# Optimization experiments

Hardware: AMD Instinct MI355X
Metric: run time of the kernel (lower is better)

## Reference

```python
import jax, jax.numpy as jnp
import numpy as np

N_NODES = 100000
N_EDGES = 3200000
N_GRAPHS = 64
NODE_FEATS = 32
LATENT = [32, 32, 32, 1]
OUT_DIM = 128
TOTAL_LATENT = sum(LATENT)  # 97


def setup_inputs() -> dict:
    key = jax.random.key(0)
    ks = jax.random.split(key, 16)
    node_feat = jax.random.normal(ks[0], (N_NODES, NODE_FEATS), dtype=jnp.float32)
    src = jax.random.randint(ks[1], (N_EDGES,), 0, N_NODES)
    dst = jax.random.randint(ks[2], (N_EDGES,), 0, N_NODES)
    graph_ids = jnp.sort(jax.random.randint(ks[3], (N_NODES,), 0, N_GRAPHS))
    # layer weights: Linear(in, out) -> W [in, out], b [out]
    dims = [NODE_FEATS] + LATENT
    inp = {
        'node_feat': node_feat,
        'src': src,
        'dst': dst,
        'graph_ids': graph_ids,
        'num_graphs': N_GRAPHS,
    }
    for i in range(len(LATENT)):
        inp[f'W{i}'] = 0.1 * jax.random.normal(ks[4 + 2 * i], (dims[i], dims[i + 1]), dtype=jnp.float32)
        inp[f'b{i}'] = 0.1 * jax.random.normal(ks[5 + 2 * i], (dims[i + 1],), dtype=jnp.float32)
    inp['Wout'] = 0.1 * jax.random.normal(ks[12], (TOTAL_LATENT, OUT_DIM), dtype=jnp.float32)
    inp['bout'] = 0.1 * jax.random.normal(ks[13], (OUT_DIM,), dtype=jnp.float32)
    return inp


def reference(node_feat, W0, b0, W1, b1, W2, b2, W3, b3, Wout, bout,
              src, dst, graph_ids, num_graphs):
    N = node_feat.shape[0]
    # node_degs = deg + 1 (adjacency row sums + 1)
    degs = jax.ops.segment_sum(jnp.ones_like(dst, dtype=node_feat.dtype), dst, num_segments=N)
    node_degs = (degs + 1.0)[:, None]  # [N, 1]

    params = [(W0, b0), (W1, b1), (W2, b2), (W3, b3)]
    h = node_feat
    cats = []
    for W, b in params:
        # n2npool = A @ h + h  (sparse SpMM via edge-list segment sum)
        agg = jax.ops.segment_sum(h[src], dst, num_segments=N) + h
        h = jnp.tanh((agg @ W + b) / node_degs)
        cats.append(h)
    hcat = jnp.concatenate(cats, axis=1)  # [N, 97]

    # per-graph sum pooling
    pooled = jax.ops.segment_sum(hcat, graph_ids, num_segments=num_graphs)  # [G, 97]
    # relu(relu(linear)) == relu(linear)
    out = jax.nn.relu(pooled @ Wout + bout)
    return out
```

## Files before the change

### kernel.cpp

```cpp
#include <hip/hip_runtime.h>
#include <hip/hip_bf16.h>


#define NFEAT 32
#define TOTLAT 97
#define NGRAPH 64
#define OUTDIM 128
#define BSHIFT 9
#define NPB 512
#define MAXBUCK 256
#define CH 8192

__device__ __forceinline__ float ftanh(float x) {
    x = fminf(fmaxf(x, -15.0f), 15.0f);
    float t = __expf(2.0f * x);
    return (t - 1.0f) / (t + 1.0f);
}

__global__ __launch_bounds__(256) void hist_kernel(const int* __restrict__ dst,
                                                   int* __restrict__ bucket_cnt,
                                                   int E, int nbuck) {
    __shared__ int h[MAXBUCK];
    for (int i = threadIdx.x; i < nbuck; i += blockDim.x) h[i] = 0;
    __syncthreads();
    int e0 = blockIdx.x * CH, e1 = min(e0 + CH, E);
    const int4* d4 = (const int4*)dst;
    int k0 = e0 >> 2, nk = (e1 - e0) >> 2;
    for (int k = k0 + threadIdx.x; k < k0 + nk; k += blockDim.x) {
        int4 v = d4[k];
        atomicAdd(&h[v.x >> BSHIFT], 1);
        atomicAdd(&h[v.y >> BSHIFT], 1);
        atomicAdd(&h[v.z >> BSHIFT], 1);
        atomicAdd(&h[v.w >> BSHIFT], 1);
    }
    for (int e = e0 + (nk << 2) + threadIdx.x; e < e1; e += blockDim.x)
        atomicAdd(&h[dst[e] >> BSHIFT], 1);
    __syncthreads();
    for (int i = threadIdx.x; i < nbuck; i += blockDim.x)
        if (h[i]) atomicAdd(&bucket_cnt[i], h[i]);
}

__global__ void bucket_scan_kernel(const int* __restrict__ bucket_cnt,
                                   int* __restrict__ bucket_start,
                                   int* __restrict__ bucket_cursor,
                                   int* __restrict__ row_ptr,
                                   int N, int E, int nbuck) {
    __shared__ int s[MAXBUCK];
    int i = threadIdx.x;
    int v = (i < nbuck) ? bucket_cnt[i] : 0;
    s[i] = v;
    __syncthreads();
    for (int d = 1; d < MAXBUCK; d <<= 1) {
        int t = (i >= d) ? s[i - d] : 0;
        __syncthreads();
        if (i >= d) s[i] += t;
        __syncthreads();
    }
    if (i < nbuck) {
        int excl = s[i] - v;
        bucket_start[i] = excl;
        bucket_cursor[i] = excl;
    }
    if (i == 0) { bucket_start[nbuck] = E; row_ptr[N] = E; }
}

__global__ __launch_bounds__(256) void part_kernel(const int* __restrict__ src,
                                                   const int* __restrict__ dst,
                                                   int* __restrict__ bucket_cursor,
                                                   int2* __restrict__ pairs,
                                                   int E, int nbuck) {
    __shared__ int h[MAXBUCK];
    __shared__ int gb[MAXBUCK];
    for (int i = threadIdx.x; i < nbuck; i += blockDim.x) h[i] = 0;
    __syncthreads();
    int e0 = blockIdx.x * CH, e1 = min(e0 + CH, E);
    const int4* d4 = (const int4*)dst;
    const int4* s4 = (const int4*)src;
    int k0 = e0 >> 2, nk = (e1 - e0) >> 2;
    for (int k = k0 + threadIdx.x; k < k0 + nk; k += blockDim.x) {
        int4 v = d4[k];
        atomicAdd(&h[v.x >> BSHIFT], 1);
        atomicAdd(&h[v.y >> BSHIFT], 1);
        atomicAdd(&h[v.z >> BSHIFT], 1);
        atomicAdd(&h[v.w >> BSHIFT], 1);
    }
    for (int e = e0 + (nk << 2) + threadIdx.x; e < e1; e += blockDim.x)
        atomicAdd(&h[dst[e] >> BSHIFT], 1);
    __syncthreads();
    for (int i = threadIdx.x; i < nbuck; i += blockDim.x) {
        int c = h[i];
        gb[i] = c ? atomicAdd(&bucket_cursor[i], c) : 0;
        h[i] = 0;
    }
    __syncthreads();
    for (int k = k0 + threadIdx.x; k < k0 + nk; k += blockDim.x) {
        int4 d = d4[k];
        int4 s = s4[k];
        int b, r;
        b = d.x >> BSHIFT; r = atomicAdd(&h[b], 1); pairs[gb[b] + r] = make_int2(s.x, d.x);
        b = d.y >> BSHIFT; r = atomicAdd(&h[b], 1); pairs[gb[b] + r] = make_int2(s.y, d.y);
        b = d.z >> BSHIFT; r = atomicAdd(&h[b], 1); pairs[gb[b] + r] = make_int2(s.z, d.z);
        b = d.w >> BSHIFT; r = atomicAdd(&h[b], 1); pairs[gb[b] + r] = make_int2(s.w, d.w);
    }
    for (int e = e0 + (nk << 2) + threadIdx.x; e < e1; e += blockDim.x) {
        int dv = dst[e];
        int b = dv >> BSHIFT;
        int r = atomicAdd(&h[b], 1);
        pairs[gb[b] + r] = make_int2(src[e], dv);
    }
}

__global__ __launch_bounds__(NPB) void csr_kernel(const int2* __restrict__ pairs,
                                                  const int* __restrict__ bucket_start,
                                                  int* __restrict__ row_ptr,
                                                  int* __restrict__ col_idx,
                                                  float* __restrict__ inv_deg, int N) {
    __shared__ int deg[NPB];
    __shared__ int scn[NPB];
    int b = blockIdx.x;
    int n0 = b << BSHIFT;
    int tid = threadIdx.x;
    deg[tid] = 0;
    __syncthreads();
    int e0 = bucket_start[b], e1 = bucket_start[b + 1];
    for (int e = e0 + tid; e < e1; e += NPB) {
        int2 p = pairs[e];
        atomicAdd(&deg[p.y - n0], 1);
    }
    __syncthreads();
    int v = deg[tid];
    scn[tid] = v;
    __syncthreads();
    for (int d = 1; d < NPB; d <<= 1) {
        int t = (tid >= d) ? scn[tid - d] : 0;
        __syncthreads();
        if (tid >= d) scn[tid] += t;
        __syncthreads();
    }
    int excl = scn[tid] - v;
    int n = n0 + tid;
    if (n < N) {
        row_ptr[n] = e0 + excl;
        inv_deg[n] = 1.0f / ((float)v + 1.0f);
    }
    deg[tid] = excl;
    __syncthreads();
    for (int e = e0 + tid; e < e1; e += NPB) {
        int2 p = pairs[e];
        int r = atomicAdd(&deg[p.y - n0], 1);
        col_idx[e0 + r] = p.x;
    }
}

template <bool WRITE_Y>
__global__ __launch_bounds__(256, 8) void layer_fused(
    const float* __restrict__ h_in, float* __restrict__ h_out,
    const float* __restrict__ W, const float* __restrict__ bvec,
    const int* __restrict__ row_ptr, const int* __restrict__ col_idx,
    const float* __restrict__ inv_deg,
    const float* __restrict__ W3, float* __restrict__ y, int N)
{
    __shared__ float accs[32][33];
    const int t = blockIdx.x * blockDim.x + threadIdx.x;
    int n = t >> 3;
    const int l8 = t & 7;
    const bool valid = n < N;
    if (!valid) n = N - 1;

    const float4* __restrict__ h4 = (const float4*)h_in;

    int beg = row_ptr[n];
    int end = row_ptr[n + 1];
    int len = end - beg;
    float4 self = h4[(size_t)n * 8 + l8];
    float4 acc = self;

    for (int e = beg; e < end; e += 32) {
        int base = e + l8 * 4;
        int my0 = __builtin_nontemporal_load(&col_idx[base + 0]);
        int my1 = __builtin_nontemporal_load(&col_idx[base + 1]);
        int my2 = __builtin_nontemporal_load(&col_idx[base + 2]);
        int my3 = __builtin_nontemporal_load(&col_idx[base + 3]);
        int rem = end - e;
#pragma unroll
        for (int sl = 0; sl < 8; ++sl) {
            int i0 = __shfl(my0, sl, 8);
            int i1 = __shfl(my1, sl, 8);
            int i2 = __shfl(my2, sl, 8);
            int i3 = __shfl(my3, sl, 8);
            int j = sl * 4;
            i0 = (j + 0 < rem) ? i0 : n;
            i1 = (j + 1 < rem) ? i1 : n;
            i2 = (j + 2 < rem) ? i2 : n;
            i3 = (j + 3 < rem) ? i3 : n;
            float4 v0 = h4[(size_t)i0 * 8 + l8];
            float4 v1 = h4[(size_t)i1 * 8 + l8];
            float4 v2 = h4[(size_t)i2 * 8 + l8];
            float4 v3 = h4[(size_t)i3 * 8 + l8];
            acc.x += v0.x + v1.x + v2.x + v3.x;
            acc.y += v0.y + v1.y + v2.y + v3.y;
            acc.z += v0.z + v1.z + v2.z + v3.z;
            acc.w += v0.w + v1.w + v2.w + v3.w;
        }
    }
    float fk = (float)(((len + 31) & ~31) - len);
    acc.x -= fk * self.x; acc.y -= fk * self.y;
    acc.z -= fk * self.z; acc.w -= fk * self.w;

    const int gl = threadIdx.x >> 3;
    const int f0 = l8 * 4;
    accs[gl][f0 + 0] = acc.x;
    accs[gl][f0 + 1] = acc.y;
    accs[gl][f0 + 2] = acc.z;
    accs[gl][f0 + 3] = acc.w;

    float4 o = *(const float4*)&bvec[f0];
#pragma unroll 8
    for (int k = 0; k < NFEAT; ++k) {
        float a = accs[gl][k];
        float4 w = *(const float4*)&W[k * NFEAT + f0];
        o.x += a * w.x; o.y += a * w.y; o.z += a * w.z; o.w += a * w.w;
    }
    float ideg = inv_deg[n];
    float4 v;
    v.x = ftanh(o.x * ideg);
    v.y = ftanh(o.y * ideg);
    v.z = ftanh(o.z * ideg);
    v.w = ftanh(o.w * ideg);

    if (valid) {
        *(float4*)&h_out[(size_t)n * NFEAT + f0] = v;
        if (WRITE_Y) {
            float4 wv = *(const float4*)&W3[f0];
            float p = v.x * wv.x + v.y * wv.y + v.z * wv.z + v.w * wv.w;
            p += __shfl_xor(p, 1);
            p += __shfl_xor(p, 2);
            p += __shfl_xor(p, 4);
            if (l8 == 0) y[n] = p;
        }
    }
}

__global__ __launch_bounds__(256) void agg3_kernel(
    const float* __restrict__ y, const float* __restrict__ b3,
    const int* __restrict__ row_ptr, const int* __restrict__ col_idx,
    const float* __restrict__ inv_deg, float* __restrict__ z, int N)
{
    int n = blockIdx.x * blockDim.x + threadIdx.x;
    if (n >= N) return;

    int beg = row_ptr[n];
    int end = row_ptr[n + 1];
    float s = y[n];
    int e = beg;
    for (; e + 8 <= end; e += 8) {
        float a0 = y[col_idx[e + 0]];
        float a1 = y[col_idx[e + 1]];
        float a2 = y[col_idx[e + 2]];
        float a3 = y[col_idx[e + 3]];
        float a4 = y[col_idx[e + 4]];
        float a5 = y[col_idx[e + 5]];
        float a6 = y[col_idx[e + 6]];
        float a7 = y[col_idx[e + 7]];
        s += ((a0 + a1) + (a2 + a3)) + ((a4 + a5) + (a6 + a7));
    }
    for (; e < end; ++e)
        s += y[col_idx[e]];

    z[n] = ftanh((s + b3[0]) * inv_deg[n]);
}

__global__ __launch_bounds__(128) void pool_kernel(
    const float* __restrict__ h0, const float* __restrict__ h1,
    const float* __restrict__ h2, const float* __restrict__ z,
    const int* __restrict__ graph_ids, float* __restrict__ pooled, int N)
{
    __shared__ int sb[2];
    int g = blockIdx.x >> 2, q = blockIdx.x & 3;
    if (threadIdx.x == 0) {
        int lo = 0, hi = N;
        while (lo < hi) { int m = (lo + hi) >> 1; if (graph_ids[m] < g) lo = m + 1; else hi = m; }
        sb[0] = lo;
        lo = 0; hi = N;
        while (lo < hi) { int m = (lo + hi) >> 1; if (graph_ids[m] < g + 1) lo = m + 1; else hi = m; }
        sb[1] = lo;
    }
    __syncthreads();
    int s = sb[0], e = sb[1];
    int per = (e - s + 3) >> 2;
    int ns = s + q * per;
    int ne = min(ns + per, e);
    int c = threadIdx.x;
    if (c >= TOTLAT || ns >= ne) return;

    float sum = 0.0f;
    if (c < 32) {
        const float* p = h0 + c;
#pragma unroll 4
        for (int n = ns; n < ne; ++n) sum += p[(size_t)n * NFEAT];
    } else if (c < 64) {
        const float* p = h1 + (c - 32);
#pragma unroll 4
        for (int n = ns; n < ne; ++n) sum += p[(size_t)n * NFEAT];
    } else if (c < 96) {
        const float* p = h2 + (c - 64);
#pragma unroll 4
        for (int n = ns; n < ne; ++n) sum += p[(size_t)n * NFEAT];
    } else {
#pragma unroll 4
        for (int n = ns; n < ne; ++n) sum += z[n];
    }
    atomicAdd(&pooled[g * TOTLAT + c], sum);
}

__global__ void final_kernel(const float* __restrict__ pooled, const float* __restrict__ Wout,
                             const float* __restrict__ bout, float* __restrict__ out) {
    int g = blockIdx.x;
    int o = threadIdx.x;
    float s = bout[o];
#pragma unroll 4
    for (int k = 0; k < TOTLAT; ++k)
        s += pooled[g * TOTLAT + k] * Wout[k * OUTDIM + o];
    out[g * OUTDIM + o] = fmaxf(s, 0.0f);
}

extern "C" void kernel_launch(void* const* d_in, const int* in_sizes, int n_in,
                              void* d_out, int out_size, void* d_ws, size_t ws_size,
                              hipStream_t stream) {
    const float* node_feat = (const float*)d_in[0];
    const int*   src       = (const int*)d_in[1];
    const int*   dst       = (const int*)d_in[2];
    const int*   graph_ids = (const int*)d_in[3];
    const float* W0 = (const float*)d_in[5];
    const float* b0 = (const float*)d_in[6];
    const float* W1 = (const float*)d_in[7];
    const float* b1 = (const float*)d_in[8];
    const float* W2 = (const float*)d_in[9];
    const float* b2 = (const float*)d_in[10];
    const float* W3 = (const float*)d_in[11];
    const float* b3 = (const float*)d_in[12];
    const float* Wout = (const float*)d_in[13];
    const float* bout = (const float*)d_in[14];
    float* out = (float*)d_out;

    const int N = in_sizes[0] / NFEAT;
    const int E = in_sizes[1];
    const int nbuck = (N + NPB - 1) >> BSHIFT;

    char* ws = (char*)d_ws;
    size_t off = 0;
    auto carve = [&](size_t bytes) -> void* {
        void* p = ws + off;
        off = (off + bytes + 255) & ~(size_t)255;
        return p;
    };
    int*   bucket_cnt    = (int*)carve((size_t)MAXBUCK * 4);
    int*   bucket_start  = (int*)carve((size_t)(MAXBUCK + 1) * 4);
    int*   bucket_cursor = (int*)carve((size_t)MAXBUCK * 4);
    int*   row_ptr       = (int*)carve((size_t)(N + 1) * 4);
    int*   col_idx       = (int*)carve((size_t)(E + 32) * 4);
    float* inv_deg       = (float*)carve((size_t)N * 4);
    float* hA            = (float*)carve((size_t)N * NFEAT * 4);
    float* hB            = (float*)carve((size_t)N * NFEAT * 4);
    float* hC            = (float*)carve((size_t)N * NFEAT * 4);
    float* y             = (float*)carve((size_t)N * 4);
    float* z             = (float*)carve((size_t)N * 4);
    float* pooled        = (float*)carve((size_t)NGRAPH * TOTLAT * 4);
    int2*  pairs         = (int2*)hA;

    hipMemsetAsync(bucket_cnt, 0, (size_t)MAXBUCK * 4, stream);
    hipMemsetAsync(pooled, 0, (size_t)NGRAPH * TOTLAT * 4, stream);

    const int nchunks = (E + CH - 1) / CH;
    hist_kernel<<<nchunks, 256, 0, stream>>>(dst, bucket_cnt, E, nbuck);
    bucket_scan_kernel<<<1, MAXBUCK, 0, stream>>>(bucket_cnt, bucket_start, bucket_cursor,
                                                  row_ptr, N, E, nbuck);
    part_kernel<<<nchunks, 256, 0, stream>>>(src, dst, bucket_cursor, pairs, E, nbuck);
    csr_kernel<<<nbuck, NPB, 0, stream>>>(pairs, bucket_start, row_ptr, col_idx, inv_deg, N);

    const int lblocks = (N * 8 + 255) / 256;
    layer_fused<false><<<lblocks, 256, 0, stream>>>(node_feat, hA, W0, b0, row_ptr, col_idx,
                                                    inv_deg, nullptr, nullptr, N);
    layer_fused<false><<<lblocks, 256, 0, stream>>>(hA, hB, W1, b1, row_ptr, col_idx,
                                                    inv_deg, nullptr, nullptr, N);
    layer_fused<true><<<lblocks, 256, 0, stream>>>(hB, hC, W2, b2, row_ptr, col_idx,
                                                   inv_deg, W3, y, N);
    agg3_kernel<<<(N + 255) / 256, 256, 0, stream>>>(y, b3, row_ptr, col_idx, inv_deg, z, N);

    pool_kernel<<<NGRAPH * 4, 128, 0, stream>>>(hA, hB, hC, z, graph_ids, pooled, N);
    final_kernel<<<NGRAPH, OUTDIM, 0, stream>>>(pooled, Wout, bout, out);
}
```

Before: 520.5 us.

## Gather neighbor features in bf16 and pack edge pairs into 32-bit words

```diff
diff --git a/kernel.cpp b/kernel.cpp
--- a/kernel.cpp
+++ b/kernel.cpp
@@ -15,6 +15,23 @@
     x = fminf(fmaxf(x, -15.0f), 15.0f);
     float t = __expf(2.0f * x);
     return (t - 1.0f) / (t + 1.0f);
+}
+__device__ __forceinline__ unsigned short f2b(float f) {
+    unsigned int x = __float_as_uint(f);
+    return (unsigned short)((x + 0x7FFFu + ((x >> 16) & 1u)) >> 16);
+}
+__device__ __forceinline__ float b2f(unsigned short u) {
+    return __uint_as_float(((unsigned int)u) << 16);
+}
+
+__global__ __launch_bounds__(256) void conv_kernel(const float* __restrict__ in,
+                                                   unsigned short* __restrict__ outb, int total4) {
+    int i = blockIdx.x * blockDim.x + threadIdx.x;
+    if (i >= total4) return;
+    float4 v = ((const float4*)in)[i];
+    ushort4 o;
+    o.x = f2b(v.x); o.y = f2b(v.y); o.z = f2b(v.z); o.w = f2b(v.w);
+    ((ushort4*)outb)[i] = o;
 }
 
 __global__ __launch_bounds__(256) void hist_kernel(const int* __restrict__ dst,
@@ -67,7 +84,7 @@
 __global__ __launch_bounds__(256) void part_kernel(const int* __restrict__ src,
                                                    const int* __restrict__ dst,
                                                    int* __restrict__ bucket_cursor,
-                                                   int2* __restrict__ pairs,
+                                                   int* __restrict__ pairs,
                                                    int E, int nbuck) {
     __shared__ int h[MAXBUCK];
     __shared__ int gb[MAXBUCK];
@@ -97,20 +114,20 @@
         int4 d = d4[k];
         int4 s = s4[k];
         int b, r;
-        b = d.x >> BSHIFT; r = atomicAdd(&h[b], 1); pairs[gb[b] + r] = make_int2(s.x, d.x);
-        b = d.y >> BSHIFT; r = atomicAdd(&h[b], 1); pairs[gb[b] + r] = make_int2(s.y, d.y);
-        b = d.z >> BSHIFT; r = atomicAdd(&h[b], 1); pairs[gb[b] + r] = make_int2(s.z, d.z);
-        b = d.w >> BSHIFT; r = atomicAdd(&h[b], 1); pairs[gb[b] + r] = make_int2(s.w, d.w);
+        b = d.x >> BSHIFT; r = atomicAdd(&h[b], 1); pairs[gb[b] + r] = s.x | ((d.x & 511) << 17);
+        b = d.y >> BSHIFT; r = atomicAdd(&h[b], 1); pairs[gb[b] + r] = s.y | ((d.y & 511) << 17);
+        b = d.z >> BSHIFT; r = atomicAdd(&h[b], 1); pairs[gb[b] + r] = s.z | ((d.z & 511) << 17);
+        b = d.w >> BSHIFT; r = atomicAdd(&h[b], 1); pairs[gb[b] + r] = s.w | ((d.w & 511) << 17);
     }
     for (int e = e0 + (nk << 2) + threadIdx.x; e < e1; e += blockDim.x) {
         int dv = dst[e];
         int b = dv >> BSHIFT;
         int r = atomicAdd(&h[b], 1);
-        pairs[gb[b] + r] = make_int2(src[e], dv);
-    }
-}
-
-__global__ __launch_bounds__(NPB) void csr_kernel(const int2* __restrict__ pairs,
+        pairs[gb[b] + r] = src[e] | ((dv & 511) << 17);
+    }
+}
+
+__global__ __launch_bounds__(NPB) void csr_kernel(const int* __restrict__ pairs,
                                                   const int* __restrict__ bucket_start,
                                                   int* __restrict__ row_ptr,
                                                   int* __restrict__ col_idx,
@@ -118,14 +135,13 @@
     __shared__ int deg[NPB];
     __shared__ int scn[NPB];
     int b = blockIdx.x;
-    int n0 = b << BSHIFT;
     int tid = threadIdx.x;
     deg[tid] = 0;
     __syncthreads();
     int e0 = bucket_start[b], e1 = bucket_start[b + 1];
     for (int e = e0 + tid; e < e1; e += NPB) {
-        int2 p = pairs[e];
-        atomicAdd(&deg[p.y - n0], 1);
+        int p = pairs[e];
+        atomicAdd(&deg[((unsigned)p) >> 17], 1);
     }
     __syncthreads();
     int v = deg[tid];
@@ -138,7 +154,7 @@
         __syncthreads();
     }
     int excl = scn[tid] - v;
-    int n = n0 + tid;
+    int n = (b << BSHIFT) + tid;
     if (n < N) {
         row_ptr[n] = e0 + excl;
         inv_deg[n] = 1.0f / ((float)v + 1.0f);
@@ -146,15 +162,16 @@
     deg[tid] = excl;
     __syncthreads();
     for (int e = e0 + tid; e < e1; e += NPB) {
-        int2 p = pairs[e];
-        int r = atomicAdd(&deg[p.y - n0], 1);
-        col_idx[e0 + r] = p.x;
-    }
-}
-
-template <bool WRITE_Y>
+        int p = pairs[e];
+        int r = atomicAdd(&deg[((unsigned)p) >> 17], 1);
+        col_idx[e0 + r] = p & 0x1FFFF;
+    }
+}
+
+template <bool WRITE_B, bool WRITE_Y>
 __global__ __launch_bounds__(256, 8) void layer_fused(
-    const float* __restrict__ h_in, float* __restrict__ h_out,
+    const float* __restrict__ h_in, const unsigned short* __restrict__ hb_in,
+    float* __restrict__ h_out, unsigned short* __restrict__ hb_out,
     const float* __restrict__ W, const float* __restrict__ bvec,
     const int* __restrict__ row_ptr, const int* __restrict__ col_idx,
     const float* __restrict__ inv_deg,
@@ -168,11 +185,13 @@
     if (!valid) n = N - 1;
 
     const float4* __restrict__ h4 = (const float4*)h_in;
+    const ushort4* __restrict__ hb4 = (const ushort4*)hb_in;
 
     int beg = row_ptr[n];
     int end = row_ptr[n + 1];
     int len = end - beg;
     float4 self = h4[(size_t)n * 8 + l8];
+    ushort4 sb = hb4[(size_t)n * 8 + l8];
     float4 acc = self;
 
     for (int e = beg; e < end; e += 32) {
@@ -193,19 +212,19 @@
             i1 = (j + 1 < rem) ? i1 : n;
             i2 = (j + 2 < rem) ? i2 : n;
             i3 = (j + 3 < rem) ? i3 : n;
-            float4 v0 = h4[(size_t)i0 * 8 + l8];
-            float4 v1 = h4[(size_t)i1 * 8 + l8];
-            float4 v2 = h4[(size_t)i2 * 8 + l8];
-            float4 v3 = h4[(size_t)i3 * 8 + l8];
-            acc.x += v0.x + v1.x + v2.x + v3.x;
-            acc.y += v0.y + v1.y + v2.y + v3.y;
-            acc.z += v0.z + v1.z + v2.z + v3.z;
-            acc.w += v0.w + v1.w + v2.w + v3.w;
+            ushort4 v0 = hb4[(size_t)i0 * 8 + l8];
+            ushort4 v1 = hb4[(size_t)i1 * 8 + l8];
+            ushort4 v2 = hb4[(size_t)i2 * 8 + l8];
+            ushort4 v3 = hb4[(size_t)i3 * 8 + l8];
+            acc.x += b2f(v0.x) + b2f(v1.x) + b2f(v2.x) + b2f(v3.x);
+            acc.y += b2f(v0.y) + b2f(v1.y) + b2f(v2.y) + b2f(v3.y);
+            acc.z += b2f(v0.z) + b2f(v1.z) + b2f(v2.z) + b2f(v3.z);
+            acc.w += b2f(v0.w) + b2f(v1.w) + b2f(v2.w) + b2f(v3.w);
         }
     }
     float fk = (float)(((len + 31) & ~31) - len);
-    acc.x -= fk * self.x; acc.y -= fk * self.y;
-    acc.z -= fk * self.z; acc.w -= fk * self.w;
+    acc.x -= fk * b2f(sb.x); acc.y -= fk * b2f(sb.y);
+    acc.z -= fk * b2f(sb.z); acc.w -= fk * b2f(sb.w);
 
     const int gl = threadIdx.x >> 3;
     const int f0 = l8 * 4;
@@ -230,6 +249,11 @@
 
     if (valid) {
         *(float4*)&h_out[(size_t)n * NFEAT + f0] = v;
+        if (WRITE_B) {
+            ushort4 ob;
+            ob.x = f2b(v.x); ob.y = f2b(v.y); ob.z = f2b(v.z); ob.w = f2b(v.w);
+            ((ushort4*)hb_out)[(size_t)n * 8 + l8] = ob;
+        }
         if (WRITE_Y) {
             float4 wv = *(const float4*)&W3[f0];
             float p = v.x * wv.x + v.y * wv.y + v.z * wv.z + v.w * wv.w;
@@ -354,22 +378,27 @@
         off = (off + bytes + 255) & ~(size_t)255;
         return p;
     };
-    int*   bucket_cnt    = (int*)carve((size_t)MAXBUCK * 4);
-    int*   bucket_start  = (int*)carve((size_t)(MAXBUCK + 1) * 4);
-    int*   bucket_cursor = (int*)carve((size_t)MAXBUCK * 4);
-    int*   row_ptr       = (int*)carve((size_t)(N + 1) * 4);
-    int*   col_idx       = (int*)carve((size_t)(E + 32) * 4);
-    float* inv_deg       = (float*)carve((size_t)N * 4);
-    float* hA            = (float*)carve((size_t)N * NFEAT * 4);
-    float* hB            = (float*)carve((size_t)N * NFEAT * 4);
-    float* hC            = (float*)carve((size_t)N * NFEAT * 4);
-    float* y             = (float*)carve((size_t)N * 4);
-    float* z             = (float*)carve((size_t)N * 4);
-    float* pooled        = (float*)carve((size_t)NGRAPH * TOTLAT * 4);
-    int2*  pairs         = (int2*)hA;
+    int*            bucket_cnt    = (int*)carve((size_t)MAXBUCK * 4);
+    int*            bucket_start  = (int*)carve((size_t)(MAXBUCK + 1) * 4);
+    int*            bucket_cursor = (int*)carve((size_t)MAXBUCK * 4);
+    int*            row_ptr       = (int*)carve((size_t)(N + 1) * 4);
+    int*            col_idx       = (int*)carve((size_t)(E + 32) * 4);
+    float*          inv_deg       = (float*)carve((size_t)N * 4);
+    float*          hA            = (float*)carve((size_t)N * NFEAT * 4);
+    float*          hB            = (float*)carve((size_t)N * NFEAT * 4);
+    float*          hC            = (float*)carve((size_t)N * NFEAT * 4);
+    unsigned short* nfb           = (unsigned short*)carve((size_t)N * NFEAT * 2);
+    unsigned short* hAb           = (unsigned short*)carve((size_t)N * NFEAT * 2);
+    unsigned short* hBb           = (unsigned short*)carve((size_t)N * NFEAT * 2);
+    float*          y             = (float*)carve((size_t)N * 4);
+    float*          z             = (float*)carve((size_t)N * 4);
+    float*          pooled        = (float*)carve((size_t)NGRAPH * TOTLAT * 4);
+    int*            pairs         = (int*)hA;
 
     hipMemsetAsync(bucket_cnt, 0, (size_t)MAXBUCK * 4, stream);
     hipMemsetAsync(pooled, 0, (size_t)NGRAPH * TOTLAT * 4, stream);
+
+    conv_kernel<<<(N * NFEAT / 4 + 255) / 256, 256, 0, stream>>>(node_feat, nfb, N * NFEAT / 4);
 
     const int nchunks = (E + CH - 1) / CH;
     hist_kernel<<<nchunks, 256, 0, stream>>>(dst, bucket_cnt, E, nbuck);
@@ -379,12 +408,15 @@
     csr_kernel<<<nbuck, NPB, 0, stream>>>(pairs, bucket_start, row_ptr, col_idx, inv_deg, N);
 
     const int lblocks = (N * 8 + 255) / 256;
-    layer_fused<false><<<lblocks, 256, 0, stream>>>(node_feat, hA, W0, b0, row_ptr, col_idx,
-                                                    inv_deg, nullptr, nullptr, N);
-    layer_fused<false><<<lblocks, 256, 0, stream>>>(hA, hB, W1, b1, row_ptr, col_idx,
-                                                    inv_deg, nullptr, nullptr, N);
-    layer_fused<true><<<lblocks, 256, 0, stream>>>(hB, hC, W2, b2, row_ptr, col_idx,
-                                                   inv_deg, W3, y, N);
+    layer_fused<true, false><<<lblocks, 256, 0, stream>>>(node_feat, nfb, hA, hAb, W0, b0,
+                                                          row_ptr, col_idx, inv_deg,
+                                                          nullptr, nullptr, N);
+    layer_fused<true, false><<<lblocks, 256, 0, stream>>>(hA, hAb, hB, hBb, W1, b1,
+                                                          row_ptr, col_idx, inv_deg,
+                                                          nullptr, nullptr, N);
+    layer_fused<false, true><<<lblocks, 256, 0, stream>>>(hB, hBb, hC, nullptr, W2, b2,
+                                                          row_ptr, col_idx, inv_deg,
+                                                          W3, y, N);
     agg3_kernel<<<(N + 255) / 256, 256, 0, stream>>>(y, b3, row_ptr, col_idx, inv_deg, z, N);
 
     pool_kernel<<<NGRAPH * 4, 128, 0, stream>>>(hA, hB, hC, z, graph_ids, pooled, N);
```

Measured after the change: 720.0 us. 38.3% more time.
